# Optimization experiments

Measured on AMD Instinct MI355X. Metric: run time of the kernel, lower is better.

## Reference

```python
import jax, jax.numpy as jnp
import numpy as np

N_NODES = 50000
N_EDGES = 800000
IN_C, HID_C, OUT_C = 128, 128, 64


def setup_inputs() -> dict:
    key = jax.random.key(0)
    ks = jax.random.split(key, 8)
    x = jax.random.normal(ks[0], (N_NODES, IN_C), dtype=jnp.float32)
    edge_index = jax.random.randint(ks[1], (2, N_EDGES), 0, N_NODES, dtype=jnp.int64)
    def glorot(k, shape):
        lim = np.sqrt(6.0 / (shape[0] + shape[1])).astype(np.float32)
        return jax.random.uniform(k, shape, jnp.float32, -lim, lim)
    return {
        "x": x,
        "edge_index": edge_index,
        "W1l": glorot(ks[2], (IN_C, HID_C)),
        "b1": jnp.zeros((HID_C,), jnp.float32),
        "W1r": glorot(ks[3], (IN_C, HID_C)),
        "W2l": glorot(ks[4], (HID_C, OUT_C)),
        "b2": jnp.zeros((OUT_C,), jnp.float32),
        "W2r": glorot(ks[5], (HID_C, OUT_C)),
    }


def _sage_conv(h, src, dst, Wl, bl, Wr):
    # mean aggregation over incoming edges (source -> target)
    n = h.shape[0]
    msg_sum = jax.ops.segment_sum(h[src], dst, num_segments=n)          # [N, d]
    deg = jax.ops.segment_sum(jnp.ones((src.shape[0],), h.dtype), dst, num_segments=n)
    agg = msg_sum / jnp.maximum(deg, 1.0)[:, None]                      # zero-degree -> 0
    # lin_l(agg) + lin_r(h); lin_l carries the bias (PyG SAGEConv default)
    return agg @ Wl + bl + h @ Wr


def reference(x, edge_index, W1l, b1, W1r, W2l, b2, W2r):
    src, dst = edge_index[0], edge_index[1]
    h = jax.nn.relu(_sage_conv(x, src, dst, W1l, b1, W1r))
    # eval-mode forward: dropout is identity
    out = _sage_conv(h, src, dst, W2l, b2, W2r)
    return out
```

## Files before the change

kernel.cpp:

```cpp
#include <hip/hip_runtime.h>

#define N_NODES 50000
#define N_EDGES 800000
#define IN_C    128
#define HID_C   128
#define OUT_C   64
#define NBUCK   196
#define BCAP    6144
#define EPB     2048
#define EBLKS   ((N_EDGES + EPB - 1) / EPB)
#define PACK_BLKS 192
#define MM1_BLKS  ((N_NODES + 63) / 64)
#define HS_STRIDE 136

typedef unsigned short ushort_t;
typedef unsigned int   uint_t;
typedef unsigned char  uchar_t;
typedef __attribute__((ext_vector_type(8))) short bf16x8;
typedef __attribute__((ext_vector_type(4))) float f32x4;
typedef __attribute__((ext_vector_type(2))) float f32x2;

__device__ inline ushort_t f2bf(float f) {
    uint_t u = __float_as_uint(f);
    uint_t r = (u + 0x7fffu + ((u >> 16) & 1u)) >> 16;
    return (ushort_t)r;
}
__device__ inline float bflo(uint_t v) { return __uint_as_float(v << 16); }
__device__ inline float bfhi(uint_t v) { return __uint_as_float(v & 0xffff0000u); }

__device__ inline void pack_one(const float* W, ushort_t* Wp, int K, int N, int idx) {
    const int j  = idx & 7;
    const int L  = (idx >> 3) & 63;
    const int t  = idx >> 9;
    const int KT = K / 32;
    const int kt = t % KT;
    const int ct = t / KT;
    const int k  = kt * 32 + (L >> 4) * 8 + j;
    const int n  = ct * 16 + (L & 15);
    Wp[idx] = f2bf(W[k * N + n]);
}

__global__ __launch_bounds__(256) void k0_kernel(
    const float* __restrict__ W1l, const float* __restrict__ W1r,
    const float* __restrict__ W2l, const float* __restrict__ W2r,
    ushort_t* __restrict__ wpack, int* __restrict__ gcur)
{
    const int b = blockIdx.x;
    if (b < PACK_BLKS) {
        const int tid = b * 256 + threadIdx.x;
        if (tid < 16384)      pack_one(W1l, wpack,          IN_C,  HID_C, tid);
        else if (tid < 32768) pack_one(W1r, wpack + 16384,  IN_C,  HID_C, tid - 16384);
        else if (tid < 40960) pack_one(W2l, wpack + 32768,  HID_C, OUT_C, tid - 32768);
        else if (tid < 49152) pack_one(W2r, wpack + 40960,  HID_C, OUT_C, tid - 40960);
    } else {
        if (threadIdx.x < NBUCK) gcur[threadIdx.x] = 0;
    }
}

__device__ inline void mm1_body(int bid, const float* __restrict__ x,
                                const ushort_t* __restrict__ wpack,
                                uchar_t* __restrict__ p1f, ushort_t* __restrict__ t1b)
{
    const int wave = threadIdx.x >> 6;
    const int lane = threadIdx.x & 63;
    const int quad = lane >> 4;
    const int m    = lane & 15;
    const int row0 = bid * 64 + wave * 16;
    const int arow = min(row0 + m, N_NODES - 1);

    const bf16x8* Bl = (const bf16x8*)(wpack);
    const bf16x8* Br = (const bf16x8*)(wpack + 16384);

    f32x4 accl[8], accr[8];
#pragma unroll
    for (int ct = 0; ct < 8; ++ct) { accl[ct] = (f32x4)(0.0f); accr[ct] = (f32x4)(0.0f); }

#pragma unroll
    for (int kt = 0; kt < 4; ++kt) {
        const float* xp = x + (size_t)arow * IN_C + kt * 32 + quad * 8;
        const float4 a0 = *(const float4*)(xp);
        const float4 a1 = *(const float4*)(xp + 4);
        bf16x8 af;
        af[0] = (short)f2bf(a0.x); af[1] = (short)f2bf(a0.y);
        af[2] = (short)f2bf(a0.z); af[3] = (short)f2bf(a0.w);
        af[4] = (short)f2bf(a1.x); af[5] = (short)f2bf(a1.y);
        af[6] = (short)f2bf(a1.z); af[7] = (short)f2bf(a1.w);
#pragma unroll
        for (int ct = 0; ct < 8; ++ct) {
            const bf16x8 bl = Bl[(ct * 4 + kt) * 64 + lane];
            const bf16x8 br = Br[(ct * 4 + kt) * 64 + lane];
            accl[ct] = __builtin_amdgcn_mfma_f32_16x16x32_bf16(af, bl, accl[ct], 0, 0, 0);
            accr[ct] = __builtin_amdgcn_mfma_f32_16x16x32_bf16(af, br, accr[ct], 0, 0, 0);
        }
    }

#pragma unroll
    for (int r = 0; r < 4; ++r) {
        const int orow = row0 + quad * 4 + r;
        if (orow < N_NODES) {
#pragma unroll
            for (int ct = 0; ct < 8; ++ct) {
                const int col = ct * 16 + m;
                const float v = accl[ct][r];
                const int pk = __builtin_amdgcn_cvt_pk_fp8_f32(v, v, 0, false);
                p1f[(size_t)orow * HID_C + col] = (uchar_t)(pk & 0xff);
                t1b[(size_t)orow * HID_C + col] = f2bf(accr[ct][r]);
            }
        }
    }
}

__global__ __launch_bounds__(256) void k1_kernel(
    const float* __restrict__ x, const ushort_t* __restrict__ wpack,
    uchar_t* __restrict__ p1f, ushort_t* __restrict__ t1b,
    const int* __restrict__ src, const int* __restrict__ dst,
    int* gcur, int* __restrict__ ebuf)
{
    __shared__ int lh[256], gbase[256], lcur[256];
    const int b = blockIdx.x;
    if (b < MM1_BLKS) {
        mm1_body(b, x, wpack, p1f, t1b);
        return;
    }
    const int blk = b - MM1_BLKS;
    const int t = threadIdx.x;
    lh[t] = 0;
    __syncthreads();
    const int base = blk * EPB;
    int v8[8], b8[8];
#pragma unroll
    for (int j = 0; j < 8; ++j) {
        const int e = base + t + j * 256;
        if (e < N_EDGES) {
            const int s = src[e], d = dst[e];
            b8[j] = d >> 8;
            v8[j] = (s << 8) | (d & 255);
            atomicAdd(&lh[b8[j]], 1);
        } else b8[j] = -1;
    }
    __syncthreads();
    if (t < NBUCK) {
        const int run = lh[t];
        gbase[t] = (run > 0) ? atomicAdd(&gcur[t], run) : 0;
        lcur[t] = 0;
    }
    __syncthreads();
#pragma unroll
    for (int j = 0; j < 8; ++j) {
        const int bk = b8[j];
        if (bk >= 0) {
            const int p = atomicAdd(&lcur[bk], 1);
            ebuf[bk * BCAP + gbase[bk] + p] = v8[j];
        }
    }
}

__global__ __launch_bounds__(256) void fill_kernel(
    const int* __restrict__ ebuf, const int* __restrict__ gcur,
    int* __restrict__ cnt, int* __restrict__ row_ptr, int* __restrict__ csr)
{
    __shared__ int lh[256], loff[256], lcur[256];
    const int b = blockIdx.x;
    const int t = threadIdx.x;
    const int e0 = b * BCAP;
    const int nb = gcur[b];
    lh[t] = 0;
    __syncthreads();
    for (int i = t; i < nb; i += 256) atomicAdd(&lh[ebuf[e0 + i] & 255], 1);
    __syncthreads();
    const int v = lh[t];
    loff[t] = v;
    __syncthreads();
    for (int off = 1; off < 256; off <<= 1) {
        const int add = (t >= off) ? loff[t - off] : 0;
        __syncthreads();
        loff[t] += add;
        __syncthreads();
    }
    const int ex = loff[t] - v;
    const int node = b * 256 + t;
    if (node < N_NODES) { cnt[node] = v; row_ptr[node] = e0 + ex; }
    lcur[t] = ex;
    __syncthreads();
    for (int i = t; i < nb; i += 256) {
        const int pr = ebuf[e0 + i];
        const int p = atomicAdd(&lcur[pr & 255], 1);
        csr[e0 + p] = pr >> 8;
    }
}

__global__ __launch_bounds__(256) void l2f_kernel(
    const uchar_t* __restrict__ p1f, const ushort_t* __restrict__ t1b,
    const float* __restrict__ b1, const int* __restrict__ row_ptr,
    const int* __restrict__ cnt, const int* __restrict__ csr,
    const ushort_t* __restrict__ wpack,
    ushort_t* __restrict__ p2b, ushort_t* __restrict__ t2b)
{
    __shared__ ushort_t hs[64 * HS_STRIDE];
    const int blk = blockIdx.x;
    const int wv  = threadIdx.x >> 6;
    const int g   = (threadIdx.x >> 4) & 3;
    const int c8  = threadIdx.x & 15;
    const uint2* p1v = (const uint2*)p1f;

#pragma unroll
    for (int p = 0; p < 4; ++p) {
        const int nl   = p * 16 + wv * 4 + g;
        const int node = blk * 64 + nl;
        float a0=0,a1=0,a2=0,a3=0,a4=0,a5=0,a6=0,a7=0;
        int degi = 0;
        if (node < N_NODES) {
            const int start = row_ptr[node];
            degi = cnt[node];
            int e = 0;
            for (; e + 3 < degi; e += 4) {
                const int s0 = csr[start + e];
                const int s1 = csr[start + e + 1];
                const int s2 = csr[start + e + 2];
                const int s3 = csr[start + e + 3];
                const uint2 v0 = p1v[(size_t)s0 * 16 + c8];
                const uint2 v1 = p1v[(size_t)s1 * 16 + c8];
                const uint2 v2 = p1v[(size_t)s2 * 16 + c8];
                const uint2 v3 = p1v[(size_t)s3 * 16 + c8];
#pragma unroll
                for (int q = 0; q < 4; ++q) {
                    const uint2 v = (q == 0) ? v0 : (q == 1) ? v1 : (q == 2) ? v2 : v3;
                    const f32x2 lx = __builtin_amdgcn_cvt_pk_f32_fp8((int)v.x, false);
                    const f32x2 hx = __builtin_amdgcn_cvt_pk_f32_fp8((int)v.x, true);
                    const f32x2 ly = __builtin_amdgcn_cvt_pk_f32_fp8((int)v.y, false);
                    const f32x2 hy = __builtin_amdgcn_cvt_pk_f32_fp8((int)v.y, true);
                    a0 += lx.x; a1 += lx.y; a2 += hx.x; a3 += hx.y;
                    a4 += ly.x; a5 += ly.y; a6 += hy.x; a7 += hy.y;
                }
            }
            for (; e < degi; ++e) {
                const uint2 v = p1v[(size_t)csr[start + e] * 16 + c8];
                const f32x2 lx = __builtin_amdgcn_cvt_pk_f32_fp8((int)v.x, false);
                const f32x2 hx = __builtin_amdgcn_cvt_pk_f32_fp8((int)v.x, true);
                const f32x2 ly = __builtin_amdgcn_cvt_pk_f32_fp8((int)v.y, false);
                const f32x2 hy = __builtin_amdgcn_cvt_pk_f32_fp8((int)v.y, true);
                a0 += lx.x; a1 += lx.y; a2 += hx.x; a3 += hx.y;
                a4 += ly.x; a5 += ly.y; a6 += hy.x; a7 += hy.y;
            }
        }
        uint4 o = make_uint4(0u, 0u, 0u, 0u);
        if (node < N_NODES) {
            const float inv = 1.0f / fmaxf((float)degi, 1.0f);
            const size_t i = (size_t)node * HID_C + c8 * 8;
            const uint4 tv = *(const uint4*)(t1b + i);
            const float4 bL = *(const float4*)(b1 + c8 * 8);
            const float4 bH = *(const float4*)(b1 + c8 * 8 + 4);
            const float r0 = fmaxf(fmaf(a0, inv, bL.x + bflo(tv.x)), 0.0f);
            const float r1 = fmaxf(fmaf(a1, inv, bL.y + bfhi(tv.x)), 0.0f);
            const float r2 = fmaxf(fmaf(a2, inv, bL.z + bflo(tv.y)), 0.0f);
            const float r3 = fmaxf(fmaf(a3, inv, bL.w + bfhi(tv.y)), 0.0f);
            const float r4 = fmaxf(fmaf(a4, inv, bH.x + bflo(tv.z)), 0.0f);
            const float r5 = fmaxf(fmaf(a5, inv, bH.y + bfhi(tv.z)), 0.0f);
            const float r6 = fmaxf(fmaf(a6, inv, bH.z + bflo(tv.w)), 0.0f);
            const float r7 = fmaxf(fmaf(a7, inv, bH.w + bfhi(tv.w)), 0.0f);
            o.x = (uint_t)f2bf(r0) | ((uint_t)f2bf(r1) << 16);
            o.y = (uint_t)f2bf(r2) | ((uint_t)f2bf(r3) << 16);
            o.z = (uint_t)f2bf(r4) | ((uint_t)f2bf(r5) << 16);
            o.w = (uint_t)f2bf(r6) | ((uint_t)f2bf(r7) << 16);
        }
        *(uint4*)&hs[nl * HS_STRIDE + c8 * 8] = o;
    }
    __syncthreads();

    const int lane = threadIdx.x & 63;
    const int quad = lane >> 4;
    const int m    = lane & 15;
    const int row0 = blk * 64 + wv * 16;

    const bf16x8* Bl = (const bf16x8*)(wpack + 32768);
    const bf16x8* Br = (const bf16x8*)(wpack + 40960);

    f32x4 accl[4], accr[4];
#pragma unroll
    for (int ct = 0; ct < 4; ++ct) { accl[ct] = (f32x4)(0.0f); accr[ct] = (f32x4)(0.0f); }

#pragma unroll
    for (int kt = 0; kt < 4; ++kt) {
        const bf16x8 af = *(const bf16x8*)&hs[(wv * 16 + m) * HS_STRIDE + kt * 32 + quad * 8];
#pragma unroll
        for (int ct = 0; ct < 4; ++ct) {
            const bf16x8 bl = Bl[(ct * 4 + kt) * 64 + lane];
            const bf16x8 br = Br[(ct * 4 + kt) * 64 + lane];
            accl[ct] = __builtin_amdgcn_mfma_f32_16x16x32_bf16(af, bl, accl[ct], 0, 0, 0);
            accr[ct] = __builtin_amdgcn_mfma_f32_16x16x32_bf16(af, br, accr[ct], 0, 0, 0);
        }
    }

#pragma unroll
    for (int r = 0; r < 4; ++r) {
        const int orow = row0 + quad * 4 + r;
        if (orow < N_NODES) {
#pragma unroll
            for (int ct = 0; ct < 4; ++ct) {
                const int col = ct * 16 + m;
                p2b[(size_t)orow * OUT_C + col] = f2bf(accl[ct][r]);
                t2b[(size_t)orow * OUT_C + col] = f2bf(accr[ct][r]);
            }
        }
    }
}

__global__ __launch_bounds__(256) void agg2_kernel(
    const ushort_t* __restrict__ p2b, const ushort_t* __restrict__ t2b,
    const float* __restrict__ b2, const int* __restrict__ row_ptr,
    const int* __restrict__ cnt, const int* __restrict__ csr,
    float* __restrict__ out)
{
    const int wv  = threadIdx.x >> 6;
    const int g   = (threadIdx.x >> 4) & 3;
    const int c4  = threadIdx.x & 15;
    const int node = blockIdx.x * 16 + wv * 4 + g;
    const int start = row_ptr[node];
    const int degi  = cnt[node];
    const uint2* p2v = (const uint2*)p2b;

    float a0 = 0.0f, a1 = 0.0f, a2 = 0.0f, a3 = 0.0f;
    int e = 0;
    for (; e + 3 < degi; e += 4) {
        const int s0 = csr[start + e];
        const int s1 = csr[start + e + 1];
        const int s2 = csr[start + e + 2];
        const int s3 = csr[start + e + 3];
        const uint2 v0 = p2v[(size_t)s0 * 16 + c4];
        const uint2 v1 = p2v[(size_t)s1 * 16 + c4];
        const uint2 v2 = p2v[(size_t)s2 * 16 + c4];
        const uint2 v3 = p2v[(size_t)s3 * 16 + c4];
        a0 += bflo(v0.x) + bflo(v1.x) + bflo(v2.x) + bflo(v3.x);
        a1 += bfhi(v0.x) + bfhi(v1.x) + bfhi(v2.x) + bfhi(v3.x);
        a2 += bflo(v0.y) + bflo(v1.y) + bflo(v2.y) + bflo(v3.y);
        a3 += bfhi(v0.y) + bfhi(v1.y) + bfhi(v2.y) + bfhi(v3.y);
    }
    for (; e < degi; ++e) {
        const uint2 v0 = p2v[(size_t)csr[start + e] * 16 + c4];
        a0 += bflo(v0.x); a1 += bfhi(v0.x);
        a2 += bflo(v0.y); a3 += bfhi(v0.y);
    }

    const float inv = 1.0f / fmaxf((float)degi, 1.0f);
    const size_t i = (size_t)node * OUT_C + c4 * 4;
    const uint2 tv = *(const uint2*)(t2b + i);
    const float4 bv = *(const float4*)(b2 + c4 * 4);
    float4 o;
    o.x = fmaf(a0, inv, bv.x + bflo(tv.x));
    o.y = fmaf(a1, inv, bv.y + bfhi(tv.x));
    o.z = fmaf(a2, inv, bv.z + bflo(tv.y));
    o.w = fmaf(a3, inv, bv.w + bfhi(tv.y));
    *(float4*)(out + i) = o;
}

extern "C" void kernel_launch(void* const* d_in, const int* in_sizes, int n_in,
                              void* d_out, int out_size, void* d_ws, size_t ws_size,
                              hipStream_t stream)
{
    const float* x   = (const float*)d_in[0];
    const int*   ei  = (const int*)d_in[1];
    const float* W1l = (const float*)d_in[2];
    const float* b1  = (const float*)d_in[3];
    const float* W1r = (const float*)d_in[4];
    const float* W2l = (const float*)d_in[5];
    const float* b2  = (const float*)d_in[6];
    const float* W2r = (const float*)d_in[7];
    float* out = (float*)d_out;

    const int* src = ei;
    const int* dst = ei + N_EDGES;

    const size_t NH = (size_t)N_NODES * HID_C;
    const size_t NO = (size_t)N_NODES * OUT_C;
    const size_t EB = (size_t)NBUCK * BCAP;

    char* ws = (char*)d_ws;
    ushort_t* t1b   = (ushort_t*)ws;                   ws += NH * sizeof(ushort_t);
    ushort_t* t2b   = (ushort_t*)ws;                   ws += NO * sizeof(ushort_t);
    ushort_t* p2b   = (ushort_t*)ws;                   ws += NO * sizeof(ushort_t);
    ushort_t* wpack = (ushort_t*)ws;                   ws += 49152 * sizeof(ushort_t);
    int* ebuf    = (int*)ws;                           ws += EB * sizeof(int);
    int* csr     = (int*)ws;                           ws += EB * sizeof(int);
    int* cnt     = (int*)ws;                           ws += N_NODES * sizeof(int);
    int* row_ptr = (int*)ws;                           ws += N_NODES * sizeof(int);
    int* gcur    = (int*)ws;                           ws += NBUCK * sizeof(int);
    uchar_t* p1f = (uchar_t*)ws;                       ws += NH * sizeof(uchar_t);

    const size_t need = (size_t)(ws - (char*)d_ws);
    if (ws_size < need) return;

    k0_kernel<<<PACK_BLKS + 1, 256, 0, stream>>>(W1l, W1r, W2l, W2r, wpack, gcur);
    k1_kernel<<<MM1_BLKS + EBLKS, 256, 0, stream>>>(
        x, wpack, p1f, t1b, src, dst, gcur, ebuf);
    fill_kernel<<<NBUCK, 256, 0, stream>>>(ebuf, gcur, cnt, row_ptr, csr);
    l2f_kernel<<<MM1_BLKS, 256, 0, stream>>>(
        p1f, t1b, b1, row_ptr, cnt, csr, wpack, p2b, t2b);
    agg2_kernel<<<(N_NODES + 15) / 16, 256, 0, stream>>>(
        p2b, t2b, b2, row_ptr, cnt, csr, out);
}
```

Before: 177.2 us.

## Store layer-2 messages in FP8, vectorize edge loads, add dynamic node scheduling

Layer-2 projected messages are now stored as FP8 instead of BF16, which halves the bytes gathered in the second aggregation. agg2 is restructured so 8 lanes each handle 8 channels per node. The edge-bucketing stage reads src/dst with int4 vector loads in place of strided scalar loads. l2f now takes nodes from a shared-memory atomic pool so that degree imbalance is evened out within a block. The FP8 storage of the second layer lowers output precision, and the vector loads rely on the edge count being a multiple of 8 and on 16-byte alignment.

```diff
diff --git a/kernel.cpp b/kernel.cpp
--- a/kernel.cpp
+++ b/kernel.cpp
@@ -27,6 +27,9 @@
 }
 __device__ inline float bflo(uint_t v) { return __uint_as_float(v << 16); }
 __device__ inline float bfhi(uint_t v) { return __uint_as_float(v & 0xffff0000u); }
+__device__ inline uchar_t f2fp8(float v) {
+    return (uchar_t)(__builtin_amdgcn_cvt_pk_fp8_f32(v, v, 0, false) & 0xff);
+}
 
 __device__ inline void pack_one(const float* W, ushort_t* Wp, int K, int N, int idx) {
     const int j  = idx & 7;
@@ -101,9 +104,7 @@
 #pragma unroll
             for (int ct = 0; ct < 8; ++ct) {
                 const int col = ct * 16 + m;
-                const float v = accl[ct][r];
-                const int pk = __builtin_amdgcn_cvt_pk_fp8_f32(v, v, 0, false);
-                p1f[(size_t)orow * HID_C + col] = (uchar_t)(pk & 0xff);
+                p1f[(size_t)orow * HID_C + col] = f2fp8(accl[ct][r]);
                 t1b[(size_t)orow * HID_C + col] = f2bf(accr[ct][r]);
             }
         }
@@ -126,17 +127,24 @@
     const int t = threadIdx.x;
     lh[t] = 0;
     __syncthreads();
-    const int base = blk * EPB;
+    const int e0 = blk * EPB + t * 8;
     int v8[8], b8[8];
-#pragma unroll
-    for (int j = 0; j < 8; ++j) {
-        const int e = base + t + j * 256;
-        if (e < N_EDGES) {
-            const int s = src[e], d = dst[e];
-            b8[j] = d >> 8;
-            v8[j] = (s << 8) | (d & 255);
+    if (e0 < N_EDGES) {
+        const int4 sa = *(const int4*)&src[e0];
+        const int4 sb = *(const int4*)&src[e0 + 4];
+        const int4 da = *(const int4*)&dst[e0];
+        const int4 db = *(const int4*)&dst[e0 + 4];
+        const int s8a[8] = {sa.x, sa.y, sa.z, sa.w, sb.x, sb.y, sb.z, sb.w};
+        const int d8a[8] = {da.x, da.y, da.z, da.w, db.x, db.y, db.z, db.w};
+#pragma unroll
+        for (int j = 0; j < 8; ++j) {
+            b8[j] = d8a[j] >> 8;
+            v8[j] = (s8a[j] << 8) | (d8a[j] & 255);
             atomicAdd(&lh[b8[j]], 1);
-        } else b8[j] = -1;
+        }
+    } else {
+#pragma unroll
+        for (int j = 0; j < 8; ++j) b8[j] = -1;
     }
     __syncthreads();
     if (t < NBUCK) {
@@ -194,24 +202,30 @@
     const float* __restrict__ b1, const int* __restrict__ row_ptr,
     const int* __restrict__ cnt, const int* __restrict__ csr,
     const ushort_t* __restrict__ wpack,
-    ushort_t* __restrict__ p2b, ushort_t* __restrict__ t2b)
+    uchar_t* __restrict__ p2f, ushort_t* __restrict__ t2b)
 {
     __shared__ ushort_t hs[64 * HS_STRIDE];
-    const int blk = blockIdx.x;
-    const int wv  = threadIdx.x >> 6;
-    const int g   = (threadIdx.x >> 4) & 3;
-    const int c8  = threadIdx.x & 15;
+    __shared__ int pool;
+    if (threadIdx.x == 0) pool = 0;
+    __syncthreads();
+
+    const int blk   = blockIdx.x;
+    const int lanew = threadIdx.x & 63;
+    const int gb    = lanew & 48;
+    const int c8    = threadIdx.x & 15;
     const uint2* p1v = (const uint2*)p1f;
 
-#pragma unroll
-    for (int p = 0; p < 4; ++p) {
-        const int nl   = p * 16 + wv * 4 + g;
+    while (true) {
+        int nl = 0;
+        if (c8 == 0) nl = atomicAdd(&pool, 1);
+        nl = __shfl(nl, gb, 64);
+        if (nl >= 64) break;
         const int node = blk * 64 + nl;
-        float a0=0,a1=0,a2=0,a3=0,a4=0,a5=0,a6=0,a7=0;
-        int degi = 0;
+        uint4 o = make_uint4(0u, 0u, 0u, 0u);
         if (node < N_NODES) {
             const int start = row_ptr[node];
-            degi = cnt[node];
+            const int degi  = cnt[node];
+            float a0=0,a1=0,a2=0,a3=0,a4=0,a5=0,a6=0,a7=0;
             int e = 0;
             for (; e + 3 < degi; e += 4) {
                 const int s0 = csr[start + e];
@@ -242,9 +256,6 @@
                 a0 += lx.x; a1 += lx.y; a2 += hx.x; a3 += hx.y;
                 a4 += ly.x; a5 += ly.y; a6 += hy.x; a7 += hy.y;
             }
-        }
-        uint4 o = make_uint4(0u, 0u, 0u, 0u);
-        if (node < N_NODES) {
             const float inv = 1.0f / fmaxf((float)degi, 1.0f);
             const size_t i = (size_t)node * HID_C + c8 * 8;
             const uint4 tv = *(const uint4*)(t1b + i);
@@ -267,6 +278,7 @@
     }
     __syncthreads();
 
+    const int wv   = threadIdx.x >> 6;
     const int lane = threadIdx.x & 63;
     const int quad = lane >> 4;
     const int m    = lane & 15;
@@ -298,7 +310,7 @@
 #pragma unroll
             for (int ct = 0; ct < 4; ++ct) {
                 const int col = ct * 16 + m;
-                p2b[(size_t)orow * OUT_C + col] = f2bf(accl[ct][r]);
+                p2f[(size_t)orow * OUT_C + col] = f2fp8(accl[ct][r]);
                 t2b[(size_t)orow * OUT_C + col] = f2bf(accr[ct][r]);
             }
         }
@@ -306,51 +318,70 @@
 }
 
 __global__ __launch_bounds__(256) void agg2_kernel(
-    const ushort_t* __restrict__ p2b, const ushort_t* __restrict__ t2b,
+    const uchar_t* __restrict__ p2f, const ushort_t* __restrict__ t2b,
     const float* __restrict__ b2, const int* __restrict__ row_ptr,
     const int* __restrict__ cnt, const int* __restrict__ csr,
     float* __restrict__ out)
 {
-    const int wv  = threadIdx.x >> 6;
-    const int g   = (threadIdx.x >> 4) & 3;
-    const int c4  = threadIdx.x & 15;
-    const int node = blockIdx.x * 16 + wv * 4 + g;
-    const int start = row_ptr[node];
-    const int degi  = cnt[node];
-    const uint2* p2v = (const uint2*)p2b;
-
-    float a0 = 0.0f, a1 = 0.0f, a2 = 0.0f, a3 = 0.0f;
-    int e = 0;
-    for (; e + 3 < degi; e += 4) {
-        const int s0 = csr[start + e];
-        const int s1 = csr[start + e + 1];
-        const int s2 = csr[start + e + 2];
-        const int s3 = csr[start + e + 3];
-        const uint2 v0 = p2v[(size_t)s0 * 16 + c4];
-        const uint2 v1 = p2v[(size_t)s1 * 16 + c4];
-        const uint2 v2 = p2v[(size_t)s2 * 16 + c4];
-        const uint2 v3 = p2v[(size_t)s3 * 16 + c4];
-        a0 += bflo(v0.x) + bflo(v1.x) + bflo(v2.x) + bflo(v3.x);
-        a1 += bfhi(v0.x) + bfhi(v1.x) + bfhi(v2.x) + bfhi(v3.x);
-        a2 += bflo(v0.y) + bflo(v1.y) + bflo(v2.y) + bflo(v3.y);
-        a3 += bfhi(v0.y) + bfhi(v1.y) + bfhi(v2.y) + bfhi(v3.y);
-    }
-    for (; e < degi; ++e) {
-        const uint2 v0 = p2v[(size_t)csr[start + e] * 16 + c4];
-        a0 += bflo(v0.x); a1 += bfhi(v0.x);
-        a2 += bflo(v0.y); a3 += bfhi(v0.y);
-    }
-
-    const float inv = 1.0f / fmaxf((float)degi, 1.0f);
-    const size_t i = (size_t)node * OUT_C + c4 * 4;
-    const uint2 tv = *(const uint2*)(t2b + i);
-    const float4 bv = *(const float4*)(b2 + c4 * 4);
-    float4 o;
-    o.x = fmaf(a0, inv, bv.x + bflo(tv.x));
-    o.y = fmaf(a1, inv, bv.y + bfhi(tv.x));
-    o.z = fmaf(a2, inv, bv.z + bflo(tv.y));
-    o.w = fmaf(a3, inv, bv.w + bfhi(tv.y));
-    *(float4*)(out + i) = o;
+    const int c8  = threadIdx.x & 7;
+    const int grp = threadIdx.x >> 3;
+    const uint2* p2v = (const uint2*)p2f;
+
+#pragma unroll
+    for (int p = 0; p < 2; ++p) {
+        const int node = blockIdx.x * 64 + p * 32 + grp;
+        if (node >= N_NODES) continue;
+        const int start = row_ptr[node];
+        const int degi  = cnt[node];
+        float a0=0,a1=0,a2=0,a3=0,a4=0,a5=0,a6=0,a7=0;
+        int e = 0;
+        for (; e + 3 < degi; e += 4) {
+            const int s0 = csr[start + e];
+            const int s1 = csr[start + e + 1];
+            const int s2 = csr[start + e + 2];
+            const int s3 = csr[start + e + 3];
+            const uint2 v0 = p2v[(size_t)s0 * 8 + c8];
+            const uint2 v1 = p2v[(size_t)s1 * 8 + c8];
+            const uint2 v2 = p2v[(size_t)s2 * 8 + c8];
+            const uint2 v3 = p2v[(size_t)s3 * 8 + c8];
+#pragma unroll
+            for (int q = 0; q < 4; ++q) {
+                const uint2 v = (q == 0) ? v0 : (q == 1) ? v1 : (q == 2) ? v2 : v3;
+                const f32x2 lx = __builtin_amdgcn_cvt_pk_f32_fp8((int)v.x, false);
+                const f32x2 hx = __builtin_amdgcn_cvt_pk_f32_fp8((int)v.x, true);
+                const f32x2 ly = __builtin_amdgcn_cvt_pk_f32_fp8((int)v.y, false);
+                const f32x2 hy = __builtin_amdgcn_cvt_pk_f32_fp8((int)v.y, true);
+                a0 += lx.x; a1 += lx.y; a2 += hx.x; a3 += hx.y;
+                a4 += ly.x; a5 += ly.y; a6 += hy.x; a7 += hy.y;
+            }
+        }
+        for (; e < degi; ++e) {
+            const uint2 v = p2v[(size_t)csr[start + e] * 8 + c8];
+            const f32x2 lx = __builtin_amdgcn_cvt_pk_f32_fp8((int)v.x, false);
+            const f32x2 hx = __builtin_amdgcn_cvt_pk_f32_fp8((int)v.x, true);
+            const f32x2 ly = __builtin_amdgcn_cvt_pk_f32_fp8((int)v.y, false);
+            const f32x2 hy = __builtin_amdgcn_cvt_pk_f32_fp8((int)v.y, true);
+            a0 += lx.x; a1 += lx.y; a2 += hx.x; a3 += hx.y;
+            a4 += ly.x; a5 += ly.y; a6 += hy.x; a7 += hy.y;
+        }
+
+        const float inv = 1.0f / fmaxf((float)degi, 1.0f);
+        const size_t i = (size_t)node * OUT_C + c8 * 8;
+        const uint4 tv = *(const uint4*)(t2b + i);
+        const float4 bL = *(const float4*)(b2 + c8 * 8);
+        const float4 bH = *(const float4*)(b2 + c8 * 8 + 4);
+        float4 oL, oH;
+        oL.x = fmaf(a0, inv, bL.x + bflo(tv.x));
+        oL.y = fmaf(a1, inv, bL.y + bfhi(tv.x));
+        oL.z = fmaf(a2, inv, bL.z + bflo(tv.y));
+        oL.w = fmaf(a3, inv, bL.w + bfhi(tv.y));
+        oH.x = fmaf(a4, inv, bH.x + bflo(tv.z));
+        oH.y = fmaf(a5, inv, bH.y + bfhi(tv.z));
+        oH.z = fmaf(a6, inv, bH.z + bflo(tv.w));
+        oH.w = fmaf(a7, inv, bH.w + bfhi(tv.w));
+        *(float4*)(out + i) = oL;
+        *(float4*)(out + i + 4) = oH;
+    }
 }
 
 extern "C" void kernel_launch(void* const* d_in, const int* in_sizes, int n_in,
@@ -377,7 +408,6 @@
     char* ws = (char*)d_ws;
     ushort_t* t1b   = (ushort_t*)ws;                   ws += NH * sizeof(ushort_t);
     ushort_t* t2b   = (ushort_t*)ws;                   ws += NO * sizeof(ushort_t);
-    ushort_t* p2b   = (ushort_t*)ws;                   ws += NO * sizeof(ushort_t);
     ushort_t* wpack = (ushort_t*)ws;                   ws += 49152 * sizeof(ushort_t);
     int* ebuf    = (int*)ws;                           ws += EB * sizeof(int);
     int* csr     = (int*)ws;                           ws += EB * sizeof(int);
@@ -385,6 +415,7 @@
     int* row_ptr = (int*)ws;                           ws += N_NODES * sizeof(int);
     int* gcur    = (int*)ws;                           ws += NBUCK * sizeof(int);
     uchar_t* p1f = (uchar_t*)ws;                       ws += NH * sizeof(uchar_t);
+    uchar_t* p2f = (uchar_t*)ws;                       ws += NO * sizeof(uchar_t);
 
     const size_t need = (size_t)(ws - (char*)d_ws);
     if (ws_size < need) return;
@@ -394,7 +425,7 @@
         x, wpack, p1f, t1b, src, dst, gcur, ebuf);
     fill_kernel<<<NBUCK, 256, 0, stream>>>(ebuf, gcur, cnt, row_ptr, csr);
     l2f_kernel<<<MM1_BLKS, 256, 0, stream>>>(
-        p1f, t1b, b1, row_ptr, cnt, csr, wpack, p2b, t2b);
-    agg2_kernel<<<(N_NODES + 15) / 16, 256, 0, stream>>>(
-        p2b, t2b, b2, row_ptr, cnt, csr, out);
-}
+        p1f, t1b, b1, row_ptr, cnt, csr, wpack, p2f, t2b);
+    agg2_kernel<<<MM1_BLKS, 256, 0, stream>>>(
+        p2f, t2b, b2, row_ptr, cnt, csr, out);
+}
```

New measurement: 175.0 us. No clear change (-1.2%).
